# Optimization experiments

Hardware: AMD Instinct MI355X
Metric: run time of the kernel (lower is better)

Reference implementation:

```python
import jax, jax.numpy as jnp
import numpy as np

N = 100000
E = 1600000
IN_FEATS = 128
N_HIDDEN = 128
N_CLASSES = 40
KLIST = [2, 2, 2]  # k=6 split over 3 layers as in DeepSGC.__init__


def setup_inputs() -> dict:
    key = jax.random.key(0)
    ks = jax.random.split(key, 10)
    features = jax.random.normal(ks[0], (N, IN_FEATS), dtype=jnp.float32)
    src = jax.random.randint(ks[1], (E,), 0, N, dtype=jnp.int64 if jax.config.jax_enable_x64 else jnp.int32)
    dst = jax.random.randint(ks[2], (E,), 0, N, dtype=jnp.int64 if jax.config.jax_enable_x64 else jnp.int32)
    def glorot(k, fan_in, fan_out):
        lim = (6.0 / (fan_in + fan_out)) ** 0.5
        return jax.random.uniform(k, (fan_in, fan_out), jnp.float32, -lim, lim)
    W1 = glorot(ks[3], IN_FEATS, N_HIDDEN)
    b1 = jnp.zeros((N_HIDDEN,), jnp.float32)
    W2 = glorot(ks[4], N_HIDDEN, N_HIDDEN)
    b2 = jnp.zeros((N_HIDDEN,), jnp.float32)
    W3 = glorot(ks[5], N_HIDDEN, N_CLASSES)
    b3 = jnp.zeros((N_CLASSES,), jnp.float32)
    return {"features": features, "src": src, "dst": dst,
            "W1": W1, "b1": b1, "W2": W2, "b2": b2, "W3": W3, "b3": b3}


def _propagate(h, src, dst, norm, k):
    # k hops of symmetric-normalized adjacency SpMM: h <- D^{-1/2} A D^{-1/2} h
    for _ in range(k):
        h = h * norm  # pre-scale [N, d]
        h = jax.ops.segment_sum(h[src], dst, num_segments=N)  # scatter-add over edges
        h = h * norm  # post-scale
    return h


def reference(features, src, dst, W1, b1, W2, b2, W3, b3):
    # in-degree based symmetric norm, clamped to >= 1 (as DGL SGConv)
    deg = jax.ops.segment_sum(jnp.ones((E,), jnp.float32), dst, num_segments=N)
    norm = jax.lax.rsqrt(jnp.clip(deg, 1.0))[:, None]  # [N, 1]

    h = features
    # layer 1: SGConv(k=2) + relu (dropout p=0 -> identity)
    h = _propagate(h, src, dst, norm, KLIST[0]) @ W1 + b1
    h = jax.nn.relu(h)
    # layer 2
    h = _propagate(h, src, dst, norm, KLIST[1]) @ W2 + b2
    h = jax.nn.relu(h)
    # layer 3 (no activation)
    h = _propagate(h, src, dst, norm, KLIST[2]) @ W3 + b3
    return h
```

## Files before the change

kernel.cpp:

```cpp
#include <hip/hip_runtime.h>
#include <hip/hip_bf16.h>


typedef __attribute__((ext_vector_type(8))) short short8v;
typedef __attribute__((ext_vector_type(4))) float f32x4;
typedef __attribute__((ext_vector_type(2))) unsigned int u32x2;

#define SBLK 128

__device__ __forceinline__ unsigned short f2bf(float x) {
    unsigned int u = __builtin_bit_cast(unsigned int, x);
    unsigned int r = u + 0x7fffu + ((u >> 16) & 1u);
    return (unsigned short)(r >> 16);
}
__device__ __forceinline__ float bf2f(unsigned short h) {
    unsigned int u = ((unsigned int)h) << 16;
    return __builtin_bit_cast(float, u);
}


__global__ void __launch_bounds__(256) deg_rank_kernel(const int* __restrict__ dst,
                                                       int* __restrict__ deg,
                                                       int* __restrict__ rank, int E) {
    int e = blockIdx.x * blockDim.x + threadIdx.x;
    if (e < E) rank[e] = atomicAdd(&deg[dst[e]], 1);
}

__global__ void __launch_bounds__(256) scanA_kernel(const int* __restrict__ deg,
                                                    int* __restrict__ rowptr,
                                                    int* __restrict__ bsum,
                                                    float* __restrict__ norm,
                                                    int n, int seg) {
    __shared__ int ws[4];
    __shared__ int carry;
    int b = blockIdx.x;
    int start = b * seg;
    int finish = start + seg; if (finish > n) finish = n;
    int t = threadIdx.x, lane = t & 63, w = t >> 6;
    if (t == 0) carry = 0;
    __syncthreads();
    for (int base = start; base < finish; base += 256) {
        int i = base + t;
        int v = 0;
        if (i < finish) {
            v = deg[i];
            norm[i] = rsqrtf((float)(v < 1 ? 1 : v));
        }
        int x = v;
        #pragma unroll
        for (int off = 1; off < 64; off <<= 1) {
            int y = __shfl_up(x, off, 64);
            if (lane >= off) x += y;
        }
        if (lane == 63) ws[w] = x;
        __syncthreads();
        int woff = 0;
        #pragma unroll
        for (int k = 0; k < 4; ++k) if (k < w) woff += ws[k];
        if (i < finish) rowptr[i] = carry + woff + x - v;
        int tot = ws[0] + ws[1] + ws[2] + ws[3];
        __syncthreads();
        if (t == 0) carry += tot;
        __syncthreads();
    }
    if (t == 0) bsum[b] = carry;
}

__global__ void __launch_bounds__(256) scanC_kernel(int* __restrict__ rowptr,
                                                    const int* __restrict__ bsum,
                                                    int n, int seg) {
    __shared__ int tmp[SBLK + 1];
    int b = blockIdx.x, t = threadIdx.x;
    if (t < SBLK) tmp[t] = bsum[t];
    __syncthreads();
    if (t == 0) {
        int s = 0;
        #pragma unroll 4
        for (int i = 0; i < SBLK; ++i) { int v = tmp[i]; tmp[i] = s; s += v; }
        tmp[SBLK] = s;
    }
    __syncthreads();
    int add = tmp[b];
    int start = b * seg;
    int finish = start + seg; if (finish > n) finish = n;
    for (int i = start + t; i < finish; i += 256) rowptr[i] += add;
    if (b == 0 && t == 0) rowptr[n] = tmp[SBLK];
}

__global__ void __launch_bounds__(256) fill_kernel(const int* __restrict__ src,
                                                   const int* __restrict__ dst,
                                                   const int* __restrict__ rowptr,
                                                   const int* __restrict__ rank,
                                                   int* __restrict__ col, int E) {
    int e = blockIdx.x * blockDim.x + threadIdx.x;
    if (e < E) col[rowptr[dst[e]] + rank[e]] = src[e];
}


__global__ void __launch_bounds__(256) xquant_kernel(const float4* __restrict__ x,
                                                     const float* __restrict__ norm,
                                                     u32x2* __restrict__ xq,
                                                     float* __restrict__ Sn,
                                                     int n) {
    int gw = (blockIdx.x * blockDim.x + threadIdx.x) >> 6;
    int lane = threadIdx.x & 63, half = lane >> 5, l32 = lane & 31;
    int node = gw * 2 + half;
    if (node >= n) return;
    float4 v = x[(size_t)node * 32 + l32];
    float m = fmaxf(fmaxf(fabsf(v.x), fabsf(v.y)), fmaxf(fabsf(v.z), fabsf(v.w)));
    #pragma unroll
    for (int s = 1; s < 32; s <<= 1) m = fmaxf(m, __shfl_xor(m, s));
    float sraw = fmaxf(m, 1e-30f);
    float inv = 32767.f / sraw;
    float sv = sraw * (1.f / 32767.f);
    int a0 = (int)rintf(fminf(fmaxf(v.x * inv, -32767.f), 32767.f));
    int a1 = (int)rintf(fminf(fmaxf(v.y * inv, -32767.f), 32767.f));
    int a2 = (int)rintf(fminf(fmaxf(v.z * inv, -32767.f), 32767.f));
    int a3 = (int)rintf(fminf(fmaxf(v.w * inv, -32767.f), 32767.f));
    u32x2 p = {(unsigned)(a0 & 0xffff) | ((unsigned)a1 << 16),
               (unsigned)(a2 & 0xffff) | ((unsigned)a3 << 16)};
    __builtin_nontemporal_store(p, &xq[(size_t)node * 32 + l32]);
    if (l32 == 0) Sn[node] = sv * norm[node];
}


template <int EPI>
__global__ void __launch_bounds__(256) spmm128_q(const u32x2* __restrict__ hq,
                                                 const float* __restrict__ esc,
                                                 const int* __restrict__ rp,
                                                 const int* __restrict__ col,
                                                 const float* __restrict__ norm,
                                                 u32x2* __restrict__ outq,
                                                 float* __restrict__ So,
                                                 u32x2* __restrict__ Hi,
                                                 u32x2* __restrict__ Lo,
                                                 int n) {
    int wid = (blockIdx.x * blockDim.x + threadIdx.x) >> 6;
    if (wid >= n) return;
    int lane = threadIdx.x & 63, half = lane >> 5, l32 = lane & 31;
    int beg = rp[wid], end = rp[wid + 1];
    f32x4 acc = {0.f, 0.f, 0.f, 0.f};
    if (beg < end) {
        int last = end - 1;
        for (int e = beg; e < end; e += 8) {
            int i0 = e + half, i1 = e + 2 + half, i2 = e + 4 + half, i3 = e + 6 + half;
            int i0c = i0 < end ? i0 : last;
            int i1c = i1 < end ? i1 : last;
            int i2c = i2 < end ? i2 : last;
            int i3c = i3 < end ? i3 : last;
            int u0 = col[i0c], u1 = col[i1c], u2 = col[i2c], u3 = col[i3c];
            float s0 = i0 < end ? esc[u0] : 0.f;
            float s1 = i1 < end ? esc[u1] : 0.f;
            float s2 = i2 < end ? esc[u2] : 0.f;
            float s3 = i3 < end ? esc[u3] : 0.f;
            u32x2 q0 = hq[(size_t)u0 * 32 + l32];
            u32x2 q1 = hq[(size_t)u1 * 32 + l32];
            u32x2 q2 = hq[(size_t)u2 * 32 + l32];
            u32x2 q3 = hq[(size_t)u3 * 32 + l32];
            acc.x += (float)(short)(q0.x) * s0;
            acc.y += (float)((int)q0.x >> 16) * s0;
            acc.z += (float)(short)(q0.y) * s0;
            acc.w += (float)((int)q0.y >> 16) * s0;
            acc.x += (float)(short)(q1.x) * s1;
            acc.y += (float)((int)q1.x >> 16) * s1;
            acc.z += (float)(short)(q1.y) * s1;
            acc.w += (float)((int)q1.y >> 16) * s1;
            acc.x += (float)(short)(q2.x) * s2;
            acc.y += (float)((int)q2.x >> 16) * s2;
            acc.z += (float)(short)(q2.y) * s2;
            acc.w += (float)((int)q2.y >> 16) * s2;
            acc.x += (float)(short)(q3.x) * s3;
            acc.y += (float)((int)q3.x >> 16) * s3;
            acc.z += (float)(short)(q3.y) * s3;
            acc.w += (float)((int)q3.y >> 16) * s3;
        }
    }
    acc.x += __shfl_xor(acc.x, 32);
    acc.y += __shfl_xor(acc.y, 32);
    acc.z += __shfl_xor(acc.z, 32);
    acc.w += __shfl_xor(acc.w, 32);
    float nv = norm[wid];
    if (EPI == 0) {
        float f = nv * nv;
        acc.x *= f; acc.y *= f; acc.z *= f; acc.w *= f;
        float m = fmaxf(fmaxf(fabsf(acc.x), fabsf(acc.y)), fmaxf(fabsf(acc.z), fabsf(acc.w)));
        #pragma unroll
        for (int s = 1; s < 64; s <<= 1) m = fmaxf(m, __shfl_xor(m, s));
        float sraw = fmaxf(m, 1e-30f);
        float inv = 32767.f / sraw;
        float sv = sraw * (1.f / 32767.f);
        if (half == 0) {
            int a0 = (int)rintf(fminf(fmaxf(acc.x * inv, -32767.f), 32767.f));
            int a1 = (int)rintf(fminf(fmaxf(acc.y * inv, -32767.f), 32767.f));
            int a2 = (int)rintf(fminf(fmaxf(acc.z * inv, -32767.f), 32767.f));
            int a3 = (int)rintf(fminf(fmaxf(acc.w * inv, -32767.f), 32767.f));
            u32x2 p = {(unsigned)(a0 & 0xffff) | ((unsigned)a1 << 16),
                       (unsigned)(a2 & 0xffff) | ((unsigned)a3 << 16)};
            __builtin_nontemporal_store(p, &outq[(size_t)wid * 32 + l32]);
        }
        if (lane == 0) So[wid] = sv;
    } else {
        if (half == 0) {
            float v0 = acc.x * nv, v1 = acc.y * nv, v2 = acc.z * nv, v3 = acc.w * nv;
            unsigned short h0 = f2bf(v0), h1 = f2bf(v1), h2 = f2bf(v2), h3 = f2bf(v3);
            unsigned short l0 = f2bf(v0 - bf2f(h0)), l1 = f2bf(v1 - bf2f(h1));
            unsigned short l2 = f2bf(v2 - bf2f(h2)), l3 = f2bf(v3 - bf2f(h3));
            u32x2 hp = {(unsigned int)h0 | ((unsigned int)h1 << 16),
                        (unsigned int)h2 | ((unsigned int)h3 << 16)};
            u32x2 lp = {(unsigned int)l0 | ((unsigned int)l1 << 16),
                        (unsigned int)l2 | ((unsigned int)l3 << 16)};
            __builtin_nontemporal_store(hp, &Hi[(size_t)wid * 32 + l32]);
            __builtin_nontemporal_store(lp, &Lo[(size_t)wid * 32 + l32]);
        }
    }
}


template <int EPI>
__global__ void __launch_bounds__(256) spmm40_q(const u32x2* __restrict__ hq,
                                                const float* __restrict__ esc,
                                                const int* __restrict__ rp,
                                                const int* __restrict__ col,
                                                const float* __restrict__ norm,
                                                u32x2* __restrict__ outq,
                                                float* __restrict__ So,
                                                f32x4* __restrict__ outf,
                                                const float* __restrict__ b3,
                                                int n) {
    int wid = (blockIdx.x * blockDim.x + threadIdx.x) >> 6;
    if (wid >= n) return;
    int lane = threadIdx.x & 63;
    int slot = lane / 10;
    int t = lane % 10;
    bool active = slot < 6;
    int beg = rp[wid], end = rp[wid + 1];
    f32x4 acc = {0.f, 0.f, 0.f, 0.f};
    if (beg < end) {
        int last = end - 1;
        for (int base = beg; base < end; base += 18) {
            float s[3];
            u32x2 q[3];
            #pragma unroll
            for (int k = 0; k < 3; ++k) {
                int i = base + 6 * k + slot;
                int ic = (active && i < end) ? i : last;
                int u = col[ic];
                s[k] = (active && i < end) ? esc[u] : 0.f;
                q[k] = hq[(size_t)u * 10 + t];
            }
            #pragma unroll
            for (int k = 0; k < 3; ++k) {
                acc.x += (float)(short)(q[k].x) * s[k];
                acc.y += (float)((int)q[k].x >> 16) * s[k];
                acc.z += (float)(short)(q[k].y) * s[k];
                acc.w += (float)((int)q[k].y >> 16) * s[k];
            }
        }
    }
    f32x4 tot = acc;
    #pragma unroll
    for (int k = 1; k < 6; ++k) {
        int srcl = t + ((slot + k) % 6) * 10;
        tot.x += __shfl(acc.x, srcl);
        tot.y += __shfl(acc.y, srcl);
        tot.z += __shfl(acc.z, srcl);
        tot.w += __shfl(acc.w, srcl);
    }
    float nv = norm[wid];
    if (EPI == 0) {
        float f = nv * nv;
        f32x4 v = {tot.x * f, tot.y * f, tot.z * f, tot.w * f};
        float m = (slot < 6)
                ? fmaxf(fmaxf(fabsf(v.x), fabsf(v.y)), fmaxf(fabsf(v.z), fabsf(v.w)))
                : 0.f;
        #pragma unroll
        for (int s = 1; s < 64; s <<= 1) m = fmaxf(m, __shfl_xor(m, s));
        float sraw = fmaxf(m, 1e-30f);
        float inv = 32767.f / sraw;
        float sv = sraw * (1.f / 32767.f);
        if (slot == 0) {
            int a0 = (int)rintf(fminf(fmaxf(v.x * inv, -32767.f), 32767.f));
            int a1 = (int)rintf(fminf(fmaxf(v.y * inv, -32767.f), 32767.f));
            int a2 = (int)rintf(fminf(fmaxf(v.z * inv, -32767.f), 32767.f));
            int a3 = (int)rintf(fminf(fmaxf(v.w * inv, -32767.f), 32767.f));
            u32x2 p = {(unsigned)(a0 & 0xffff) | ((unsigned)a1 << 16),
                       (unsigned)(a2 & 0xffff) | ((unsigned)a3 << 16)};
            __builtin_nontemporal_store(p, &outq[(size_t)wid * 10 + t]);
        }
        if (lane == 0) So[wid] = sv;
    } else {
        if (slot == 0) {
            f32x4 bv = ((const f32x4*)b3)[t];
            f32x4 o = {tot.x * nv + bv.x, tot.y * nv + bv.y,
                       tot.z * nv + bv.z, tot.w * nv + bv.w};
            __builtin_nontemporal_store(o, &outf[(size_t)wid * 10 + t]);
        }
    }
}


__device__ __forceinline__ void wprep_one(const float* __restrict__ W,
                                          short* __restrict__ Wh,
                                          short* __restrict__ Wl,
                                          int ncols, int CF, int i) {
    int j = i & 7;
    int lane = (i >> 3) & 63;
    int f = i >> 9;
    int cf = f % CF, ks = f / CF;
    int k = ks * 32 + 8 * (lane >> 4) + j;
    int c = cf * 16 + (lane & 15);
    float v = (c < ncols) ? W[k * ncols + c] : 0.f;
    unsigned short h = f2bf(v);
    unsigned short l = f2bf(v - bf2f(h));
    Wh[i] = (short)h;
    Wl[i] = (short)l;
}

__global__ void __launch_bounds__(256) wprep_all(const float* __restrict__ W1,
                                                 const float* __restrict__ W2,
                                                 const float* __restrict__ W3,
                                                 short* __restrict__ W1h, short* __restrict__ W1l,
                                                 short* __restrict__ W2h, short* __restrict__ W2l,
                                                 short* __restrict__ W3h, short* __restrict__ W3l) {
    int i = blockIdx.x * blockDim.x + threadIdx.x;
    if (i < 16384) wprep_one(W1, W1h, W1l, 128, 8, i);
    else if (i < 32768) wprep_one(W2, W2h, W2l, 128, 8, i - 16384);
    else if (i < 38912) wprep_one(W3, W3h, W3l, 40, 3, i - 32768);
}


__global__ void __launch_bounds__(256) gemm_mfma128(const unsigned short* __restrict__ Ahi,
                                                    const unsigned short* __restrict__ Alo,
                                                    const short8v* __restrict__ Wh,
                                                    const short8v* __restrict__ Wl,
                                                    const float* __restrict__ bias,
                                                    const float* __restrict__ norm,
                                                    unsigned short* __restrict__ Cq,
                                                    float* __restrict__ So,
                                                    float* __restrict__ Sno,
                                                    int n) {
    int lane = threadIdx.x & 63;
    int wid = threadIdx.x >> 6;
    int r0 = blockIdx.x * 64 + wid * 16;
    if (r0 >= n) return;
    int arow = r0 + (lane & 15);
    if (arow > n - 1) arow = n - 1;
    int kbase = 8 * (lane >> 4);
    f32x4 acc[8];
    #pragma unroll
    for (int i = 0; i < 8; ++i) acc[i] = (f32x4){0.f, 0.f, 0.f, 0.f};
    #pragma unroll
    for (int ks = 0; ks < 4; ++ks) {
        short8v ah = *(const short8v*)(Ahi + (size_t)arow * 128 + ks * 32 + kbase);
        short8v al = *(const short8v*)(Alo + (size_t)arow * 128 + ks * 32 + kbase);
        #pragma unroll
        for (int cf = 0; cf < 8; ++cf) {
            short8v bh = Wh[(ks * 8 + cf) * 64 + lane];
            short8v bl = Wl[(ks * 8 + cf) * 64 + lane];
            acc[cf] = __builtin_amdgcn_mfma_f32_16x16x32_bf16(ah, bh, acc[cf], 0, 0, 0);
            acc[cf] = __builtin_amdgcn_mfma_f32_16x16x32_bf16(al, bh, acc[cf], 0, 0, 0);
            acc[cf] = __builtin_amdgcn_mfma_f32_16x16x32_bf16(ah, bl, acc[cf], 0, 0, 0);
        }
    }
    int rbase = r0 + (lane >> 4) * 4;
    int c0 = lane & 15;
    float bc[8];
    #pragma unroll
    for (int cf = 0; cf < 8; ++cf) bc[cf] = bias[cf * 16 + c0];

    float mq[4] = {0.f, 0.f, 0.f, 0.f};
    #pragma unroll
    for (int cf = 0; cf < 8; ++cf) {
        #pragma unroll
        for (int q = 0; q < 4; ++q)
            mq[q] = fmaxf(mq[q], fmaxf(acc[cf][q] + bc[cf], 0.f));
    }
    #pragma unroll
    for (int s = 1; s < 16; s <<= 1) {
        #pragma unroll
        for (int q = 0; q < 4; ++q) mq[q] = fmaxf(mq[q], __shfl_xor(mq[q], s));
    }
    float invq[4], svq[4];
    #pragma unroll
    for (int q = 0; q < 4; ++q) {
        float sraw = fmaxf(mq[q], 1e-30f);
        invq[q] = 32767.f / sraw;
        svq[q] = sraw * (1.f / 32767.f);
    }
    #pragma unroll
    for (int cf = 0; cf < 8; ++cf) {
        int colc = cf * 16 + c0;
        #pragma unroll
        for (int q = 0; q < 4; ++q) {
            int row = rbase + q;
            if (row >= n) continue;
            float v = fmaxf(acc[cf][q] + bc[cf], 0.f);
            int qi = (int)rintf(fminf(v * invq[q], 32767.f));
            Cq[(size_t)row * 128 + colc] = (unsigned short)qi;
        }
    }
    if (c0 == 0) {
        #pragma unroll
        for (int q = 0; q < 4; ++q) {
            int row = rbase + q;
            if (row < n) { So[row] = svq[q]; Sno[row] = svq[q] * norm[row]; }
        }
    }
}

__global__ void __launch_bounds__(256) gemm_mfma40(const unsigned short* __restrict__ Aq,
                                                   const float* __restrict__ SA,
                                                   const short8v* __restrict__ Wh,
                                                   const short8v* __restrict__ Wl,
                                                   const float* __restrict__ norm,
                                                   unsigned short* __restrict__ Cq,
                                                   float* __restrict__ S3,
                                                   float* __restrict__ Sn3,
                                                   int n) {
    int lane = threadIdx.x & 63;
    int wid = threadIdx.x >> 6;
    int r0 = blockIdx.x * 64 + wid * 16;
    if (r0 >= n) return;
    int arow = r0 + (lane & 15);
    if (arow > n - 1) arow = n - 1;
    int kbase = 8 * (lane >> 4);
    float sA = SA[arow];
    f32x4 acc[3];
    #pragma unroll
    for (int i = 0; i < 3; ++i) acc[i] = (f32x4){0.f, 0.f, 0.f, 0.f};
    #pragma unroll
    for (int ks = 0; ks < 4; ++ks) {
        short8v qv = *(const short8v*)(Aq + (size_t)arow * 128 + ks * 32 + kbase);
        short8v ah, al;
        #pragma unroll
        for (int j = 0; j < 8; ++j) {
            float v = (float)qv[j] * sA;
            unsigned int uv = __builtin_bit_cast(unsigned int, v);
            unsigned short hi = (unsigned short)(uv >> 16);
            float r = v - bf2f(hi);
            ah[j] = (short)hi;
            al[j] = (short)f2bf(r);
        }
        #pragma unroll
        for (int cf = 0; cf < 3; ++cf) {
            short8v bh = Wh[(ks * 3 + cf) * 64 + lane];
            short8v bl = Wl[(ks * 3 + cf) * 64 + lane];
            acc[cf] = __builtin_amdgcn_mfma_f32_16x16x32_bf16(ah, bh, acc[cf], 0, 0, 0);
            acc[cf] = __builtin_amdgcn_mfma_f32_16x16x32_bf16(al, bh, acc[cf], 0, 0, 0);
            acc[cf] = __builtin_amdgcn_mfma_f32_16x16x32_bf16(ah, bl, acc[cf], 0, 0, 0);
        }
    }
    int rbase = r0 + (lane >> 4) * 4;
    int c0 = lane & 15;
    float mq[4] = {0.f, 0.f, 0.f, 0.f};
    #pragma unroll
    for (int cf = 0; cf < 3; ++cf) {
        int colc = cf * 16 + c0;
        if (colc < 40) {
            #pragma unroll
            for (int q = 0; q < 4; ++q) mq[q] = fmaxf(mq[q], fabsf(acc[cf][q]));
        }
    }
    #pragma unroll
    for (int s = 1; s < 16; s <<= 1) {
        #pragma unroll
        for (int q = 0; q < 4; ++q) mq[q] = fmaxf(mq[q], __shfl_xor(mq[q], s));
    }
    float invq[4], svq[4];
    #pragma unroll
    for (int q = 0; q < 4; ++q) {
        float sraw = fmaxf(mq[q], 1e-30f);
        invq[q] = 32767.f / sraw;
        svq[q] = sraw * (1.f / 32767.f);
    }
    #pragma unroll
    for (int cf = 0; cf < 3; ++cf) {
        int colc = cf * 16 + c0;
        if (colc >= 40) continue;
        #pragma unroll
        for (int q = 0; q < 4; ++q) {
            int row = rbase + q;
            if (row >= n) continue;
            float v = acc[cf][q];
            int qi = (int)rintf(fminf(fmaxf(v * invq[q], -32767.f), 32767.f));
            Cq[(size_t)row * 40 + colc] = (unsigned short)qi;
        }
    }
    if (c0 == 0) {
        #pragma unroll
        for (int q = 0; q < 4; ++q) {
            int row = rbase + q;
            if (row < n) { S3[row] = svq[q]; Sn3[row] = svq[q] * norm[row]; }
        }
    }
}


extern "C" void kernel_launch(void* const* d_in, const int* in_sizes, int n_in,
                              void* d_out, int out_size, void* d_ws, size_t ws_size,
                              hipStream_t stream) {
    const float* features = (const float*)d_in[0];
    const int*   src      = (const int*)d_in[1];
    const int*   dst      = (const int*)d_in[2];
    const float* W1 = (const float*)d_in[3];
    const float* b1 = (const float*)d_in[4];
    const float* W2 = (const float*)d_in[5];
    const float* b2 = (const float*)d_in[6];
    const float* W3 = (const float*)d_in[7];
    const float* b3 = (const float*)d_in[8];
    float* out = (float*)d_out;

    const int N = in_sizes[0] / 128;
    const int E = in_sizes[1];

    char* ws = (char*)d_ws;
    size_t off = 0;
    auto alloc = [&](size_t bytes) -> void* {
        void* p = ws + off;
        off += (bytes + 511) & ~(size_t)511;
        return p;
    };
    u32x2* QA = (u32x2*)alloc((size_t)N * 32 * sizeof(u32x2));
    u32x2* QB = (u32x2*)alloc((size_t)N * 32 * sizeof(u32x2));
    unsigned short* Hi = (unsigned short*)alloc((size_t)N * 128 * sizeof(unsigned short));
    unsigned short* Lo = (unsigned short*)alloc((size_t)N * 128 * sizeof(unsigned short));
    float* Snx = (float*)alloc((size_t)N * sizeof(float));
    float* Sk  = (float*)alloc((size_t)N * sizeof(float));
    float* Sg  = (float*)alloc((size_t)N * sizeof(float));
    float* Sng = (float*)alloc((size_t)N * sizeof(float));
    float* S3  = (float*)alloc((size_t)N * sizeof(float));
    float* Sn3 = (float*)alloc((size_t)N * sizeof(float));
    float* S4  = (float*)alloc((size_t)N * sizeof(float));
    int*   col    = (int*)alloc((size_t)E * sizeof(int));
    int*   deg    = (int*)alloc((size_t)N * sizeof(int));
    int*   rowptr = (int*)alloc((size_t)(N + 1) * sizeof(int));
    float* norm   = (float*)alloc((size_t)N * sizeof(float));
    int*   bsum   = (int*)alloc((size_t)(SBLK + 2) * sizeof(int));
    short* W1h = (short*)alloc(16384 * sizeof(short));
    short* W1l = (short*)alloc(16384 * sizeof(short));
    short* W2h = (short*)alloc(16384 * sizeof(short));
    short* W2l = (short*)alloc(16384 * sizeof(short));
    short* W3h = (short*)alloc(6144 * sizeof(short));
    short* W3l = (short*)alloc(6144 * sizeof(short));
    int*   rank = (int*)Hi;
    u32x2* G1 = (u32x2*)QB;
    u32x2* G2 = (u32x2*)Hi;

    const int seg = (N + SBLK - 1) / SBLK;
    const int eblocks = (E + 255) / 256;

    hipMemsetAsync(deg, 0, (size_t)N * sizeof(int), stream);
    deg_rank_kernel<<<eblocks, 256, 0, stream>>>(dst, deg, rank, E);
    scanA_kernel<<<SBLK, 256, 0, stream>>>(deg, rowptr, bsum, norm, N, seg);
    scanC_kernel<<<SBLK, 256, 0, stream>>>(rowptr, bsum, N, seg);
    fill_kernel<<<eblocks, 256, 0, stream>>>(src, dst, rowptr, rank, col, E);

    wprep_all<<<(38912 + 255) / 256, 256, 0, stream>>>(W1, W2, W3, W1h, W1l, W2h, W2l, W3h, W3l);
    {
        int waves2 = (N + 1) / 2;
        int xblocks = (waves2 * 64 + 255) / 256;
        xquant_kernel<<<xblocks, 256, 0, stream>>>((const float4*)features, norm, QA, Snx, N);
    }

    const int spmm_blocks = (N * 64 + 255) / 256;
    const int gemm_blocks = (N + 63) / 64;

    spmm128_q<0><<<spmm_blocks, 256, 0, stream>>>(QA, Snx, rowptr, col, norm,
                                                  QB, Sk, nullptr, nullptr, N);
    spmm128_q<1><<<spmm_blocks, 256, 0, stream>>>(QB, Sk, rowptr, col, norm,
                                                  nullptr, nullptr, (u32x2*)Hi, (u32x2*)Lo, N);
    gemm_mfma128<<<gemm_blocks, 256, 0, stream>>>(Hi, Lo, (const short8v*)W1h, (const short8v*)W1l,
                                                  b1, norm, (unsigned short*)QA, Sg, Sng, N);

    spmm128_q<0><<<spmm_blocks, 256, 0, stream>>>(QA, Sng, rowptr, col, norm,
                                                  QB, Sk, nullptr, nullptr, N);
    spmm128_q<1><<<spmm_blocks, 256, 0, stream>>>(QB, Sk, rowptr, col, norm,
                                                  nullptr, nullptr, (u32x2*)Hi, (u32x2*)Lo, N);
    gemm_mfma128<<<gemm_blocks, 256, 0, stream>>>(Hi, Lo, (const short8v*)W2h, (const short8v*)W2l,
                                                  b2, norm, (unsigned short*)QA, Sg, Sng, N);

    gemm_mfma40<<<gemm_blocks, 256, 0, stream>>>((const unsigned short*)QA, Sg,
                                                 (const short8v*)W3h, (const short8v*)W3l,
                                                 norm, (unsigned short*)G1, S3, Sn3, N);
    spmm40_q<0><<<spmm_blocks, 256, 0, stream>>>(G1, Sn3, rowptr, col, norm,
                                                 G2, S4, nullptr, nullptr, N);
    spmm40_q<1><<<spmm_blocks, 256, 0, stream>>>(G2, S4, rowptr, col, norm,
                                                 nullptr, nullptr, (f32x4*)out, b3, N);
}
```

Measured before the change: 636.1 us.

## Quantize second-hop SpMM output to int16 and dequantize inside GEMM

```diff
diff --git a/kernel.cpp b/kernel.cpp
--- a/kernel.cpp
+++ b/kernel.cpp
@@ -124,17 +124,15 @@
 }
 
 
-template <int EPI>
-__global__ void __launch_bounds__(256) spmm128_q(const u32x2* __restrict__ hq,
-                                                 const float* __restrict__ esc,
-                                                 const int* __restrict__ rp,
-                                                 const int* __restrict__ col,
-                                                 const float* __restrict__ norm,
-                                                 u32x2* __restrict__ outq,
-                                                 float* __restrict__ So,
-                                                 u32x2* __restrict__ Hi,
-                                                 u32x2* __restrict__ Lo,
-                                                 int n) {
+template <int SQ>
+__global__ void __launch_bounds__(256, 8) spmm128_q(const u32x2* __restrict__ hq,
+                                                    const float* __restrict__ esc,
+                                                    const int* __restrict__ rp,
+                                                    const int* __restrict__ col,
+                                                    const float* __restrict__ norm,
+                                                    u32x2* __restrict__ outq,
+                                                    float* __restrict__ So,
+                                                    int n) {
     int wid = (blockIdx.x * blockDim.x + threadIdx.x) >> 6;
     if (wid >= n) return;
     int lane = threadIdx.x & 63, half = lane >> 5, l32 = lane & 31;
@@ -142,21 +140,36 @@
     f32x4 acc = {0.f, 0.f, 0.f, 0.f};
     if (beg < end) {
         int last = end - 1;
-        for (int e = beg; e < end; e += 8) {
-            int i0 = e + half, i1 = e + 2 + half, i2 = e + 4 + half, i3 = e + 6 + half;
+        int u0, u1, u2, u3;
+        float s0, s1, s2, s3;
+        {
+            int i0 = beg + half, i1 = beg + 2 + half, i2 = beg + 4 + half, i3 = beg + 6 + half;
             int i0c = i0 < end ? i0 : last;
             int i1c = i1 < end ? i1 : last;
             int i2c = i2 < end ? i2 : last;
             int i3c = i3 < end ? i3 : last;
-            int u0 = col[i0c], u1 = col[i1c], u2 = col[i2c], u3 = col[i3c];
-            float s0 = i0 < end ? esc[u0] : 0.f;
-            float s1 = i1 < end ? esc[u1] : 0.f;
-            float s2 = i2 < end ? esc[u2] : 0.f;
-            float s3 = i3 < end ? esc[u3] : 0.f;
+            u0 = col[i0c]; u1 = col[i1c]; u2 = col[i2c]; u3 = col[i3c];
+            s0 = i0 < end ? esc[u0] : 0.f;
+            s1 = i1 < end ? esc[u1] : 0.f;
+            s2 = i2 < end ? esc[u2] : 0.f;
+            s3 = i3 < end ? esc[u3] : 0.f;
+        }
+        for (int e = beg; e < end; e += 8) {
             u32x2 q0 = hq[(size_t)u0 * 32 + l32];
             u32x2 q1 = hq[(size_t)u1 * 32 + l32];
             u32x2 q2 = hq[(size_t)u2 * 32 + l32];
             u32x2 q3 = hq[(size_t)u3 * 32 + l32];
+            int en = e + 8;
+            int j0 = en + half, j1 = en + 2 + half, j2 = en + 4 + half, j3 = en + 6 + half;
+            int j0c = j0 < end ? j0 : last;
+            int j1c = j1 < end ? j1 : last;
+            int j2c = j2 < end ? j2 : last;
+            int j3c = j3 < end ? j3 : last;
+            int nu0 = col[j0c], nu1 = col[j1c], nu2 = col[j2c], nu3 = col[j3c];
+            float ns0 = j0 < end ? esc[nu0] : 0.f;
+            float ns1 = j1 < end ? esc[nu1] : 0.f;
+            float ns2 = j2 < end ? esc[nu2] : 0.f;
+            float ns3 = j3 < end ? esc[nu3] : 0.f;
             acc.x += (float)(short)(q0.x) * s0;
             acc.y += (float)((int)q0.x >> 16) * s0;
             acc.z += (float)(short)(q0.y) * s0;
@@ -173,6 +186,8 @@
             acc.y += (float)((int)q3.x >> 16) * s3;
             acc.z += (float)(short)(q3.y) * s3;
             acc.w += (float)((int)q3.y >> 16) * s3;
+            u0 = nu0; u1 = nu1; u2 = nu2; u3 = nu3;
+            s0 = ns0; s1 = ns1; s2 = ns2; s3 = ns3;
         }
     }
     acc.x += __shfl_xor(acc.x, 32);
@@ -180,53 +195,38 @@
     acc.z += __shfl_xor(acc.z, 32);
     acc.w += __shfl_xor(acc.w, 32);
     float nv = norm[wid];
-    if (EPI == 0) {
-        float f = nv * nv;
-        acc.x *= f; acc.y *= f; acc.z *= f; acc.w *= f;
-        float m = fmaxf(fmaxf(fabsf(acc.x), fabsf(acc.y)), fmaxf(fabsf(acc.z), fabsf(acc.w)));
-        #pragma unroll
-        for (int s = 1; s < 64; s <<= 1) m = fmaxf(m, __shfl_xor(m, s));
-        float sraw = fmaxf(m, 1e-30f);
-        float inv = 32767.f / sraw;
-        float sv = sraw * (1.f / 32767.f);
-        if (half == 0) {
-            int a0 = (int)rintf(fminf(fmaxf(acc.x * inv, -32767.f), 32767.f));
-            int a1 = (int)rintf(fminf(fmaxf(acc.y * inv, -32767.f), 32767.f));
-            int a2 = (int)rintf(fminf(fmaxf(acc.z * inv, -32767.f), 32767.f));
-            int a3 = (int)rintf(fminf(fmaxf(acc.w * inv, -32767.f), 32767.f));
-            u32x2 p = {(unsigned)(a0 & 0xffff) | ((unsigned)a1 << 16),
-                       (unsigned)(a2 & 0xffff) | ((unsigned)a3 << 16)};
-            __builtin_nontemporal_store(p, &outq[(size_t)wid * 32 + l32]);
-        }
-        if (lane == 0) So[wid] = sv;
-    } else {
-        if (half == 0) {
-            float v0 = acc.x * nv, v1 = acc.y * nv, v2 = acc.z * nv, v3 = acc.w * nv;
-            unsigned short h0 = f2bf(v0), h1 = f2bf(v1), h2 = f2bf(v2), h3 = f2bf(v3);
-            unsigned short l0 = f2bf(v0 - bf2f(h0)), l1 = f2bf(v1 - bf2f(h1));
-            unsigned short l2 = f2bf(v2 - bf2f(h2)), l3 = f2bf(v3 - bf2f(h3));
-            u32x2 hp = {(unsigned int)h0 | ((unsigned int)h1 << 16),
-                        (unsigned int)h2 | ((unsigned int)h3 << 16)};
-            u32x2 lp = {(unsigned int)l0 | ((unsigned int)l1 << 16),
-                        (unsigned int)l2 | ((unsigned int)l3 << 16)};
-            __builtin_nontemporal_store(hp, &Hi[(size_t)wid * 32 + l32]);
-            __builtin_nontemporal_store(lp, &Lo[(size_t)wid * 32 + l32]);
-        }
-    }
+    float f = SQ ? nv * nv : nv;
+    acc.x *= f; acc.y *= f; acc.z *= f; acc.w *= f;
+    float m = fmaxf(fmaxf(fabsf(acc.x), fabsf(acc.y)), fmaxf(fabsf(acc.z), fabsf(acc.w)));
+    #pragma unroll
+    for (int s = 1; s < 64; s <<= 1) m = fmaxf(m, __shfl_xor(m, s));
+    float sraw = fmaxf(m, 1e-30f);
+    float inv = 32767.f / sraw;
+    float sv = sraw * (1.f / 32767.f);
+    if (half == 0) {
+        int a0 = (int)rintf(fminf(fmaxf(acc.x * inv, -32767.f), 32767.f));
+        int a1 = (int)rintf(fminf(fmaxf(acc.y * inv, -32767.f), 32767.f));
+        int a2 = (int)rintf(fminf(fmaxf(acc.z * inv, -32767.f), 32767.f));
+        int a3 = (int)rintf(fminf(fmaxf(acc.w * inv, -32767.f), 32767.f));
+        u32x2 p = {(unsigned)(a0 & 0xffff) | ((unsigned)a1 << 16),
+                   (unsigned)(a2 & 0xffff) | ((unsigned)a3 << 16)};
+        __builtin_nontemporal_store(p, &outq[(size_t)wid * 32 + l32]);
+    }
+    if (lane == 0) So[wid] = sv;
 }
 
 
 template <int EPI>
-__global__ void __launch_bounds__(256) spmm40_q(const u32x2* __restrict__ hq,
-                                                const float* __restrict__ esc,
-                                                const int* __restrict__ rp,
-                                                const int* __restrict__ col,
-                                                const float* __restrict__ norm,
-                                                u32x2* __restrict__ outq,
-                                                float* __restrict__ So,
-                                                f32x4* __restrict__ outf,
-                                                const float* __restrict__ b3,
-                                                int n) {
+__global__ void __launch_bounds__(256, 8) spmm40_q(const u32x2* __restrict__ hq,
+                                                   const float* __restrict__ esc,
+                                                   const int* __restrict__ rp,
+                                                   const int* __restrict__ col,
+                                                   const float* __restrict__ norm,
+                                                   u32x2* __restrict__ outq,
+                                                   float* __restrict__ So,
+                                                   f32x4* __restrict__ outf,
+                                                   const float* __restrict__ b3,
+                                                   int n) {
     int wid = (blockIdx.x * blockDim.x + threadIdx.x) >> 6;
     if (wid >= n) return;
     int lane = threadIdx.x & 63;
@@ -329,8 +329,8 @@
 }
 
 
-__global__ void __launch_bounds__(256) gemm_mfma128(const unsigned short* __restrict__ Ahi,
-                                                    const unsigned short* __restrict__ Alo,
+__global__ void __launch_bounds__(256) gemm_mfma128(const unsigned short* __restrict__ Aq,
+                                                    const float* __restrict__ SA,
                                                     const short8v* __restrict__ Wh,
                                                     const short8v* __restrict__ Wl,
                                                     const float* __restrict__ bias,
@@ -346,13 +346,23 @@
     int arow = r0 + (lane & 15);
     if (arow > n - 1) arow = n - 1;
     int kbase = 8 * (lane >> 4);
+    float sA = SA[arow];
     f32x4 acc[8];
     #pragma unroll
     for (int i = 0; i < 8; ++i) acc[i] = (f32x4){0.f, 0.f, 0.f, 0.f};
     #pragma unroll
     for (int ks = 0; ks < 4; ++ks) {
-        short8v ah = *(const short8v*)(Ahi + (size_t)arow * 128 + ks * 32 + kbase);
-        short8v al = *(const short8v*)(Alo + (size_t)arow * 128 + ks * 32 + kbase);
+        short8v qv = *(const short8v*)(Aq + (size_t)arow * 128 + ks * 32 + kbase);
+        short8v ah, al;
+        #pragma unroll
+        for (int j = 0; j < 8; ++j) {
+            float v = (float)qv[j] * sA;
+            unsigned int uv = __builtin_bit_cast(unsigned int, v);
+            unsigned short hi = (unsigned short)(uv >> 16);
+            float r = v - bf2f(hi);
+            ah[j] = (short)hi;
+            al[j] = (short)f2bf(r);
+        }
         #pragma unroll
         for (int cf = 0; cf < 8; ++cf) {
             short8v bh = Wh[(ks * 8 + cf) * 64 + lane];
@@ -522,10 +532,10 @@
     };
     u32x2* QA = (u32x2*)alloc((size_t)N * 32 * sizeof(u32x2));
     u32x2* QB = (u32x2*)alloc((size_t)N * 32 * sizeof(u32x2));
-    unsigned short* Hi = (unsigned short*)alloc((size_t)N * 128 * sizeof(unsigned short));
-    unsigned short* Lo = (unsigned short*)alloc((size_t)N * 128 * sizeof(unsigned short));
+    u32x2* QC = (u32x2*)alloc((size_t)N * 32 * sizeof(u32x2));
     float* Snx = (float*)alloc((size_t)N * sizeof(float));
     float* Sk  = (float*)alloc((size_t)N * sizeof(float));
+    float* Sq2 = (float*)alloc((size_t)N * sizeof(float));
     float* Sg  = (float*)alloc((size_t)N * sizeof(float));
     float* Sng = (float*)alloc((size_t)N * sizeof(float));
     float* S3  = (float*)alloc((size_t)N * sizeof(float));
@@ -542,9 +552,9 @@
     short* W2l = (short*)alloc(16384 * sizeof(short));
     short* W3h = (short*)alloc(6144 * sizeof(short));
     short* W3l = (short*)alloc(6144 * sizeof(short));
-    int*   rank = (int*)Hi;
+    int*   rank = (int*)QC;
     u32x2* G1 = (u32x2*)QB;
-    u32x2* G2 = (u32x2*)Hi;
+    u32x2* G2 = (u32x2*)QC;
 
     const int seg = (N + SBLK - 1) / SBLK;
     const int eblocks = (E + 255) / 256;
@@ -565,18 +575,16 @@
     const int spmm_blocks = (N * 64 + 255) / 256;
     const int gemm_blocks = (N + 63) / 64;
 
-    spmm128_q<0><<<spmm_blocks, 256, 0, stream>>>(QA, Snx, rowptr, col, norm,
-                                                  QB, Sk, nullptr, nullptr, N);
-    spmm128_q<1><<<spmm_blocks, 256, 0, stream>>>(QB, Sk, rowptr, col, norm,
-                                                  nullptr, nullptr, (u32x2*)Hi, (u32x2*)Lo, N);
-    gemm_mfma128<<<gemm_blocks, 256, 0, stream>>>(Hi, Lo, (const short8v*)W1h, (const short8v*)W1l,
+    spmm128_q<1><<<spmm_blocks, 256, 0, stream>>>(QA, Snx, rowptr, col, norm, QB, Sk, N);
+    spmm128_q<0><<<spmm_blocks, 256, 0, stream>>>(QB, Sk, rowptr, col, norm, QC, Sq2, N);
+    gemm_mfma128<<<gemm_blocks, 256, 0, stream>>>((const unsigned short*)QC, Sq2,
+                                                  (const short8v*)W1h, (const short8v*)W1l,
                                                   b1, norm, (unsigned short*)QA, Sg, Sng, N);
 
-    spmm128_q<0><<<spmm_blocks, 256, 0, stream>>>(QA, Sng, rowptr, col, norm,
-                                                  QB, Sk, nullptr, nullptr, N);
-    spmm128_q<1><<<spmm_blocks, 256, 0, stream>>>(QB, Sk, rowptr, col, norm,
-                                                  nullptr, nullptr, (u32x2*)Hi, (u32x2*)Lo, N);
-    gemm_mfma128<<<gemm_blocks, 256, 0, stream>>>(Hi, Lo, (const short8v*)W2h, (const short8v*)W2l,
+    spmm128_q<1><<<spmm_blocks, 256, 0, stream>>>(QA, Sng, rowptr, col, norm, QB, Sk, N);
+    spmm128_q<0><<<spmm_blocks, 256, 0, stream>>>(QB, Sk, rowptr, col, norm, QC, Sq2, N);
+    gemm_mfma128<<<gemm_blocks, 256, 0, stream>>>((const unsigned short*)QC, Sq2,
+                                                  (const short8v*)W2h, (const short8v*)W2l,
                                                   b2, norm, (unsigned short*)QA, Sg, Sng, N);
 
     gemm_mfma40<<<gemm_blocks, 256, 0, stream>>>((const unsigned short*)QA, Sg,
```

Result: no change. 627.2 us (-1.4%).
